# Kernel optimization log

Hardware: AMD Instinct MI355X
Metric: run time of the kernel (lower is better)

## Reference

```python
import jax, jax.numpy as jnp
import numpy as np

D_MODEL = 1024
H = 16
HEAD_DIM = D_MODEL // H  # 64


def setup_inputs() -> dict:
    key = jax.random.key(0)
    ks = jax.random.split(key, 11)
    B, S, D = 1, 4096, D_MODEL
    scale = 1.0 / np.sqrt(D)
    inp = {
        'q': jax.random.normal(ks[0], (B, S, D), jnp.float32),
        'k': jax.random.normal(ks[1], (B, S, D), jnp.float32),
        'v': jax.random.normal(ks[2], (B, S, D), jnp.float32),
        'w_q': jax.random.normal(ks[3], (D, D), jnp.float32) * scale,
        'b_q': jnp.zeros((D,), jnp.float32),
        'w_k': jax.random.normal(ks[4], (D, D), jnp.float32) * scale,
        'b_k': jnp.zeros((D,), jnp.float32),
        'w_v': jax.random.normal(ks[5], (D, D), jnp.float32) * scale,
        'b_v': jnp.zeros((D,), jnp.float32),
        'w_o': jax.random.normal(ks[6], (D, D), jnp.float32) * scale,
        'b_o': jnp.zeros((D,), jnp.float32),
    }
    return inp


def reference(q, k, v, w_q, b_q, w_k, b_k, w_v, b_v, w_o, b_o):
    B, Sq, D = q.shape
    Sk = k.shape[1]
    # Linear projections (torch Linear: x @ W.T + b), split into heads: [B,H,S,hd]
    Q = (q @ w_q.T + b_q).reshape(B, Sq, H, HEAD_DIM).transpose(0, 2, 1, 3)
    K = (k @ w_k.T + b_k).reshape(B, Sk, H, HEAD_DIM).transpose(0, 2, 1, 3)
    V = (v @ w_v.T + b_v).reshape(B, Sk, H, HEAD_DIM).transpose(0, 2, 1, 3)
    # Naive attention: full [B,H,Sq,Sk] scores, softmax, then AV
    scores = jnp.einsum('bhqd,bhkd->bhqk', Q, K) / jnp.sqrt(jnp.float32(HEAD_DIM))
    attn = jax.nn.softmax(scores, axis=-1)
    ctx = jnp.einsum('bhqk,bhkd->bhqd', attn, V)
    concat = ctx.transpose(0, 2, 1, 3).reshape(B, Sq, D)
    return concat @ w_o.T + b_o
```

## Files before the change

kernel.cpp:

```cpp
#include <hip/hip_runtime.h>
#include <stdint.h>

#define S_LEN 4096
#define DM 1024
#define NH 16

typedef __attribute__((ext_vector_type(8))) short short8;
typedef __attribute__((ext_vector_type(4))) float float4v;
typedef __attribute__((ext_vector_type(4))) unsigned short ushort4v;

typedef __attribute__((address_space(1))) const void* as1cvp;
typedef __attribute__((address_space(3))) void* as3vp;

#define MFMA16(a, b, c) __builtin_amdgcn_mfma_f32_16x16x32_bf16((a), (b), (c), 0, 0, 0)
#define GLOAD_LDS16(g, l) \
  __builtin_amdgcn_global_load_lds((as1cvp)(g), (as3vp)(l), 16, 0, 0)

__device__ __forceinline__ unsigned short f2bf(float f) {
  unsigned u = __float_as_uint(f);
  u += 0x7fffu + ((u >> 16) & 1u);
  return (unsigned short)(u >> 16);
}

__device__ __forceinline__ float exp2_hw(float x) {
  float r;
  asm("v_exp_f32 %0, %1" : "=v"(r) : "v"(x));
  return r;
}

__global__ __launch_bounds__(256) void cast_all(
    const float* __restrict__ q, const float* __restrict__ k, const float* __restrict__ v,
    const float* __restrict__ wq, const float* __restrict__ wk, const float* __restrict__ wv,
    const float* __restrict__ wo, unsigned short* __restrict__ dst)
{
  const float* src; size_t off; int n;
  switch (blockIdx.y) {
    case 0: src = q;  off = 0u;        n = 4194304; break;
    case 1: src = k;  off = 4194304u;  n = 4194304; break;
    case 2: src = v;  off = 8388608u;  n = 4194304; break;
    case 3: src = wq; off = 12582912u; n = 1048576; break;
    case 4: src = wk; off = 13631488u; n = 1048576; break;
    case 5: src = wv; off = 14680064u; n = 1048576; break;
    default: src = wo; off = 15728640u; n = 1048576; break;
  }
  int nv = n >> 2;
  for (int i = blockIdx.x * blockDim.x + threadIdx.x; i < nv; i += gridDim.x * blockDim.x) {
    float4v val = ((const float4v*)src)[i];
    ushort4v o;
    o.x = f2bf(val.x); o.y = f2bf(val.y); o.z = f2bf(val.z); o.w = f2bf(val.w);
    ((ushort4v*)(dst + off))[i] = o;
  }
}

template<int MODE>
__device__ __forceinline__ void gemm128(
    const unsigned short* __restrict__ A, const unsigned short* __restrict__ Bw,
    unsigned short* Cb, const float* __restrict__ bias, float alpha,
    unsigned short* As, unsigned short* Bs, unsigned short* T)
{
  const int K = 1024, N = 1024;
  int bm = blockIdx.x, bn = blockIdx.y;
  int t = threadIdx.x, lane = t & 63, w = t >> 6;
  int l15 = lane & 15, l4 = lane >> 4;
  int wr = w >> 1, wc = w & 1;

  float4v acc[4][4] = {};

  for (int kt = 0; kt < K / 64; ++kt) {
#pragma unroll
    for (int i = 0; i < 4; ++i) {
      int ci = i * 256 + t;
      int r = ci >> 3, cb = ci & 7;
      int lb = cb ^ (r & 7);
      GLOAD_LDS16(A + (size_t)(bm * 128 + r) * K + kt * 64 + lb * 8, As + (size_t)ci * 8);
      GLOAD_LDS16(Bw + (size_t)(bn * 128 + r) * K + kt * 64 + lb * 8, Bs + (size_t)ci * 8);
    }
    __syncthreads();
#pragma unroll
    for (int kk = 0; kk < 2; ++kk) {
      short8 af[4], bfr[4];
#pragma unroll
      for (int mf = 0; mf < 4; ++mf) {
        int row = wr * 64 + mf * 16 + l15;
        int pc = (kk * 4 + l4) ^ (row & 7);
        af[mf] = *(const short8*)&As[row * 64 + pc * 8];
      }
#pragma unroll
      for (int nf = 0; nf < 4; ++nf) {
        int row = wc * 64 + nf * 16 + l15;
        int pc = (kk * 4 + l4) ^ (row & 7);
        bfr[nf] = *(const short8*)&Bs[row * 64 + pc * 8];
      }
#pragma unroll
      for (int mf = 0; mf < 4; ++mf)
#pragma unroll
        for (int nf = 0; nf < 4; ++nf)
          acc[mf][nf] = MFMA16(af[mf], bfr[nf], acc[mf][nf]);
    }
    __syncthreads();
  }

  if (MODE == 2) {
#pragma unroll
    for (int hc = 0; hc < 2; ++hc) {
      if (wc == hc) {
#pragma unroll
        for (int mf = 0; mf < 4; ++mf)
#pragma unroll
          for (int nf = 0; nf < 4; ++nf) {
            int c = nf * 16 + l15;
            float bv = bias[bn * 128 + hc * 64 + c];
            ushort4v pk;
#pragma unroll
            for (int j = 0; j < 4; ++j) pk[j] = f2bf((acc[mf][nf][j] + bv) * alpha);
            *(ushort4v*)&T[c * 136 + wr * 64 + mf * 16 + l4 * 4] = pk;
          }
      }
      __syncthreads();
      {
        int c = t >> 2, rseg = (t & 3) * 32;
        size_t gbase = (size_t)(bn * 128 + hc * 64 + c) * S_LEN + bm * 128 + rseg;
#pragma unroll
        for (int s = 0; s < 4; ++s) {
          short8 vv = *(const short8*)&T[c * 136 + rseg + s * 8];
          *(short8*)&Cb[gbase + s * 8] = vv;
        }
      }
      __syncthreads();
    }
    return;
  }

#pragma unroll
  for (int mf = 0; mf < 4; ++mf)
#pragma unroll
    for (int nf = 0; nf < 4; ++nf) {
      int col = bn * 128 + wc * 64 + nf * 16 + l15;
      float bv = bias[col];
#pragma unroll
      for (int j = 0; j < 4; ++j) {
        int row = bm * 128 + wr * 64 + mf * 16 + l4 * 4 + j;
        Cb[(size_t)row * N + col] = f2bf((acc[mf][nf][j] + bv) * alpha);
      }
    }
}

__global__ __launch_bounds__(256) void proj_qkv(
    const unsigned short* xq, const unsigned short* xk, const unsigned short* xv,
    const unsigned short* wq, const unsigned short* wk, const unsigned short* wv,
    unsigned short* Qp, unsigned short* Kp, unsigned short* Vt,
    const float* bq, const float* bk, const float* bv)
{
  __shared__ unsigned short As[128 * 64], Bs[128 * 64];
  __shared__ unsigned short T[64 * 136];
  switch (blockIdx.z) {
    case 0:  gemm128<0>(xq, wq, Qp, bq, 0.1803368867f, As, Bs, T); break;
    case 1:  gemm128<0>(xk, wk, Kp, bk, 1.0f,          As, Bs, T); break;
    default: gemm128<2>(xv, wv, Vt, bv, 1.0f,          As, Bs, T); break;
  }
}

__global__ __launch_bounds__(256) void proj_o(
    const unsigned short* __restrict__ ctx, const unsigned short* __restrict__ wo,
    float* __restrict__ out, const float* __restrict__ bo)
{
  const int K = 1024, N = 1024;
  __shared__ unsigned short As[128 * 64], Bs[64 * 64];
  int bm = blockIdx.x, bn = blockIdx.y;
  int t = threadIdx.x, lane = t & 63, w = t >> 6;
  int l15 = lane & 15, l4 = lane >> 4;

  float4v acc[2][4] = {};

  for (int kt = 0; kt < K / 64; ++kt) {
#pragma unroll
    for (int i = 0; i < 4; ++i) {
      int ci = i * 256 + t;
      int r = ci >> 3, cb = ci & 7;
      int lb = cb ^ (r & 7);
      GLOAD_LDS16(ctx + (size_t)(bm * 128 + r) * K + kt * 64 + lb * 8, As + (size_t)ci * 8);
    }
#pragma unroll
    for (int i = 0; i < 2; ++i) {
      int ci = i * 256 + t;
      int r = ci >> 3, cb = ci & 7;
      int lb = cb ^ (r & 7);
      GLOAD_LDS16(wo + (size_t)(bn * 64 + r) * K + kt * 64 + lb * 8, Bs + (size_t)ci * 8);
    }
    __syncthreads();
#pragma unroll
    for (int kk = 0; kk < 2; ++kk) {
      short8 af[2], bfr[4];
#pragma unroll
      for (int mf = 0; mf < 2; ++mf) {
        int row = w * 32 + mf * 16 + l15;
        int pc = (kk * 4 + l4) ^ (row & 7);
        af[mf] = *(const short8*)&As[row * 64 + pc * 8];
      }
#pragma unroll
      for (int nf = 0; nf < 4; ++nf) {
        int row = nf * 16 + l15;
        int pc = (kk * 4 + l4) ^ (row & 7);
        bfr[nf] = *(const short8*)&Bs[row * 64 + pc * 8];
      }
#pragma unroll
      for (int mf = 0; mf < 2; ++mf)
#pragma unroll
        for (int nf = 0; nf < 4; ++nf)
          acc[mf][nf] = MFMA16(af[mf], bfr[nf], acc[mf][nf]);
    }
    __syncthreads();
  }

#pragma unroll
  for (int mf = 0; mf < 2; ++mf)
#pragma unroll
    for (int nf = 0; nf < 4; ++nf) {
      int col = bn * 64 + nf * 16 + l15;
      float bv = bo[col];
#pragma unroll
      for (int j = 0; j < 4; ++j) {
        int row = bm * 128 + w * 32 + mf * 16 + l4 * 4 + j;
        out[(size_t)row * N + col] = acc[mf][nf][j] + bv;
      }
    }
}

template<int BUF>
__device__ __forceinline__ void attn_tile(
    int kt,
    const unsigned short* kb0, const unsigned short* kb1,
    const unsigned short* vb0, const unsigned short* vb1,
    unsigned short* pw, const unsigned short* pr,
    const unsigned short* kg, const unsigned short* vg,
    unsigned short* kls, unsigned short* vls,
    const short8 (&qf)[2], float4v (&acc_o)[4], float& m_run, float& l_run,
    int l4)
{
  if (kt + 1 < 64) {
    GLOAD_LDS16(kg + (size_t)(kt + 1) * (64 * DM), kls + (1 - BUF) * 4096);
    GLOAD_LDS16(vg + (kt + 1) * 64, vls + (1 - BUF) * 4096);
  }

  float4v sc[4];
  __builtin_amdgcn_s_setprio(1);
#pragma unroll
  for (int nf = 0; nf < 4; ++nf) {
    short8 kf0 = *(const short8*)(kb0 + BUF * 4096 + nf * 1024);
    short8 kf1 = *(const short8*)(kb1 + BUF * 4096 + nf * 1024);
    float4v z = {0.f, 0.f, 0.f, 0.f};
    z = MFMA16(kf0, qf[0], z);
    sc[nf] = MFMA16(kf1, qf[1], z);
  }
  __builtin_amdgcn_s_setprio(0);

  float mxl = fmaxf(fmaxf(fmaxf(sc[0][0], sc[0][1]), sc[0][2]), sc[0][3]);
#pragma unroll
  for (int nf = 1; nf < 4; ++nf)
    mxl = fmaxf(fmaxf(fmaxf(fmaxf(mxl, sc[nf][0]), sc[nf][1]), sc[nf][2]), sc[nf][3]);

  if (!__all(mxl <= m_run + 11.5f)) {
    float mx = fmaxf(mxl, __shfl_xor(mxl, 16));
    mx = fmaxf(mx, __shfl_xor(mx, 32));
    float mnew = fmaxf(m_run, mx);
    float corr = exp2_hw(m_run - mnew);
    m_run = mnew;
    l_run *= corr;
#pragma unroll
    for (int j = 0; j < 4; ++j) {
      float cj = __shfl(corr, l4 * 4 + j);
#pragma unroll
      for (int nf2 = 0; nf2 < 4; ++nf2) acc_o[nf2][j] *= cj;
    }
  }

  float ps = 0.f;
#pragma unroll
  for (int nf = 0; nf < 4; ++nf) {
    float p0 = exp2_hw(sc[nf][0] - m_run);
    float p1 = exp2_hw(sc[nf][1] - m_run);
    float p2 = exp2_hw(sc[nf][2] - m_run);
    float p3 = exp2_hw(sc[nf][3] - m_run);
    ps += (p0 + p1) + (p2 + p3);
    unsigned lo, hi;
    asm("v_cvt_pk_bf16_f32 %0, %1, %2" : "=v"(lo) : "v"(p0), "v"(p1));
    asm("v_cvt_pk_bf16_f32 %0, %1, %2" : "=v"(hi) : "v"(p2), "v"(p3));
    uint2 u; u.x = lo; u.y = hi;
    *(uint2*)(pw + nf * 16) = u;
  }
  l_run += ps;

  short8 pf[2];
#pragma unroll
  for (int kc = 0; kc < 2; ++kc)
    pf[kc] = *(const short8*)(pr + kc * 32);

  __builtin_amdgcn_s_setprio(1);
#pragma unroll
  for (int nfd = 0; nfd < 4; ++nfd) {
    short8 vf0 = *(const short8*)(vb0 + BUF * 4096 + nfd * 1024);
    short8 vf1 = *(const short8*)(vb1 + BUF * 4096 + nfd * 1024);
    acc_o[nfd] = MFMA16(pf[0], vf0, acc_o[nfd]);
    acc_o[nfd] = MFMA16(pf[1], vf1, acc_o[nfd]);
  }
  __builtin_amdgcn_s_setprio(0);
  __syncthreads();
}

__global__ __launch_bounds__(512) void attn_fused(
    const unsigned short* __restrict__ Qp, const unsigned short* __restrict__ Kp,
    const unsigned short* __restrict__ Vt, unsigned short* __restrict__ ctx)
{
  __shared__ unsigned short Ks[2][64 * 64];
  __shared__ unsigned short Vts[2][64 * 64];
  __shared__ unsigned short Ps[8][16 * 72];

  int bid = blockIdx.x;
  int wg = (bid & 7) * 64 + (bid >> 3);
  int h = wg >> 5, qt = wg & 31;

  int t = threadIdx.x, lane = t & 63, w = t >> 6;
  int l15 = lane & 15, l4 = lane >> 4;

  short8 qf[2];
  int qrow0 = qt * 128 + w * 16;
#pragma unroll
  for (int ks = 0; ks < 2; ++ks)
    qf[ks] = *(const short8*)&Qp[(size_t)(qrow0 + l15) * DM + h * 64 + ks * 32 + l4 * 8];

  float4v acc_o[4] = {};
  float m_run = -INFINITY, l_run = 0.f;

  const int swz = l15 & 7;
  const unsigned short* kb0 = &Ks[0][l15 * 64 + ((l4) ^ swz) * 8];
  const unsigned short* kb1 = &Ks[0][l15 * 64 + ((4 + l4) ^ swz) * 8];
  const unsigned short* vb0 = &Vts[0][l15 * 64 + ((l4) ^ swz) * 8];
  const unsigned short* vb1 = &Vts[0][l15 * 64 + ((4 + l4) ^ swz) * 8];
  unsigned short* pw = &Ps[w][l15 * 72 + l4 * 4];
  const unsigned short* pr = &Ps[w][l15 * 72 + l4 * 8];

  int sr = t >> 3, sp = t & 7;
  int slb = sp ^ (sr & 7);
  const unsigned short* kg = Kp + (size_t)sr * DM + h * 64 + slb * 8;
  const unsigned short* vg = Vt + (size_t)(h * 64 + sr) * S_LEN + slb * 8;
  unsigned short* kls = &Ks[0][t * 8];
  unsigned short* vls = &Vts[0][t * 8];

  GLOAD_LDS16(kg, kls);
  GLOAD_LDS16(vg, vls);
  __syncthreads();

  for (int kt = 0; kt < 64; kt += 2) {
    attn_tile<0>(kt,     kb0, kb1, vb0, vb1, pw, pr, kg, vg, kls, vls, qf, acc_o, m_run, l_run, l4);
    attn_tile<1>(kt + 1, kb0, kb1, vb0, vb1, pw, pr, kg, vg, kls, vls, qf, acc_o, m_run, l_run, l4);
  }

  float lr = l_run;
  lr += __shfl_xor(lr, 16);
  lr += __shfl_xor(lr, 32);
#pragma unroll
  for (int j = 0; j < 4; ++j) {
    float lj = __shfl(lr, l4 * 4 + j);
    float inv = 1.0f / lj;
#pragma unroll
    for (int nfd = 0; nfd < 4; ++nfd) {
      int row = qrow0 + l4 * 4 + j;
      int col = h * 64 + nfd * 16 + l15;
      ctx[(size_t)row * DM + col] = f2bf(acc_o[nfd][j] * inv);
    }
  }
}

extern "C" void kernel_launch(void* const* d_in, const int* in_sizes, int n_in,
                              void* d_out, int out_size, void* d_ws, size_t ws_size,
                              hipStream_t stream) {
  const float* q  = (const float*)d_in[0];
  const float* k  = (const float*)d_in[1];
  const float* v  = (const float*)d_in[2];
  const float* wq = (const float*)d_in[3];
  const float* bq = (const float*)d_in[4];
  const float* wk = (const float*)d_in[5];
  const float* bk = (const float*)d_in[6];
  const float* wv = (const float*)d_in[7];
  const float* bv = (const float*)d_in[8];
  const float* wo = (const float*)d_in[9];
  const float* bo = (const float*)d_in[10];

  unsigned short* ws  = (unsigned short*)d_ws;
  unsigned short* qb  = ws;
  unsigned short* kb  = ws + 4194304u;
  unsigned short* vb  = ws + 8388608u;
  unsigned short* wqb = ws + 12582912u;
  unsigned short* wkb = ws + 13631488u;
  unsigned short* wvb = ws + 14680064u;
  unsigned short* wob = ws + 15728640u;
  unsigned short* Qp  = ws + 16777216u;
  unsigned short* Kp  = ws + 20971520u;
  unsigned short* Vt  = ws + 25165824u;
  unsigned short* ctx = qb;
  float* out = (float*)d_out;

  cast_all<<<dim3(1024, 7), 256, 0, stream>>>(q, k, v, wq, wk, wv, wo, ws);
  proj_qkv<<<dim3(32, 8, 3), 256, 0, stream>>>(qb, kb, vb, wqb, wkb, wvb, Qp, Kp, Vt, bq, bk, bv);
  attn_fused<<<dim3(512), 512, 0, stream>>>(Qp, Kp, Vt, ctx);
  proj_o<<<dim3(32, 16), 256, 0, stream>>>(ctx, wob, out, bo);
}
```

Baseline: 169.5 us.

## Quad-buffer K/V tiles to halve block barriers and swizzle P scratch layout

The K/V LDS staging grows from double to quad buffering. Two tiles are prefetched at a time and a block-wide barrier runs every two tiles instead of every tile, which cuts synchronisation overhead and gives loads more time to land. The per-wave P scratch drops its 72-element padding in favour of an XOR-swizzled 64-wide layout to avoid bank conflicts. LDS use roughly doubles for K/V, which could limit occupancy. P is now written and read within a wave without a barrier between tiles, which relies on wave-local ordering.

```diff
diff --git a/kernel.cpp b/kernel.cpp
--- a/kernel.cpp
+++ b/kernel.cpp
@@ -228,20 +228,13 @@
 
 template<int BUF>
 __device__ __forceinline__ void attn_tile(
-    int kt,
     const unsigned short* kb0, const unsigned short* kb1,
     const unsigned short* vb0, const unsigned short* vb1,
-    unsigned short* pw, const unsigned short* pr,
-    const unsigned short* kg, const unsigned short* vg,
-    unsigned short* kls, unsigned short* vls,
+    unsigned short* pwrow, const int (&pwo)[4],
+    const unsigned short* pr0, const unsigned short* pr1,
     const short8 (&qf)[2], float4v (&acc_o)[4], float& m_run, float& l_run,
     int l4)
 {
-  if (kt + 1 < 64) {
-    GLOAD_LDS16(kg + (size_t)(kt + 1) * (64 * DM), kls + (1 - BUF) * 4096);
-    GLOAD_LDS16(vg + (kt + 1) * 64, vls + (1 - BUF) * 4096);
-  }
-
   float4v sc[4];
   __builtin_amdgcn_s_setprio(1);
 #pragma unroll
@@ -286,14 +279,13 @@
     asm("v_cvt_pk_bf16_f32 %0, %1, %2" : "=v"(lo) : "v"(p0), "v"(p1));
     asm("v_cvt_pk_bf16_f32 %0, %1, %2" : "=v"(hi) : "v"(p2), "v"(p3));
     uint2 u; u.x = lo; u.y = hi;
-    *(uint2*)(pw + nf * 16) = u;
+    *(uint2*)(pwrow + pwo[nf]) = u;
   }
   l_run += ps;
 
   short8 pf[2];
-#pragma unroll
-  for (int kc = 0; kc < 2; ++kc)
-    pf[kc] = *(const short8*)(pr + kc * 32);
+  pf[0] = *(const short8*)pr0;
+  pf[1] = *(const short8*)pr1;
 
   __builtin_amdgcn_s_setprio(1);
 #pragma unroll
@@ -304,16 +296,15 @@
     acc_o[nfd] = MFMA16(pf[1], vf1, acc_o[nfd]);
   }
   __builtin_amdgcn_s_setprio(0);
-  __syncthreads();
 }
 
 __global__ __launch_bounds__(512) void attn_fused(
     const unsigned short* __restrict__ Qp, const unsigned short* __restrict__ Kp,
     const unsigned short* __restrict__ Vt, unsigned short* __restrict__ ctx)
 {
-  __shared__ unsigned short Ks[2][64 * 64];
-  __shared__ unsigned short Vts[2][64 * 64];
-  __shared__ unsigned short Ps[8][16 * 72];
+  __shared__ unsigned short Ks[4][64 * 64];
+  __shared__ unsigned short Vts[4][64 * 64];
+  __shared__ unsigned short Ps[8][16 * 64];
 
   int bid = blockIdx.x;
   int wg = (bid & 7) * 64 + (bid >> 3);
@@ -336,8 +327,13 @@
   const unsigned short* kb1 = &Ks[0][l15 * 64 + ((4 + l4) ^ swz) * 8];
   const unsigned short* vb0 = &Vts[0][l15 * 64 + ((l4) ^ swz) * 8];
   const unsigned short* vb1 = &Vts[0][l15 * 64 + ((4 + l4) ^ swz) * 8];
-  unsigned short* pw = &Ps[w][l15 * 72 + l4 * 4];
-  const unsigned short* pr = &Ps[w][l15 * 72 + l4 * 8];
+  unsigned short* pwrow = &Ps[w][l15 * 64];
+  int pwo[4];
+#pragma unroll
+  for (int nf = 0; nf < 4; ++nf)
+    pwo[nf] = ((2 * nf + (l4 >> 1)) ^ swz) * 8 + (l4 & 1) * 4;
+  const unsigned short* pr0 = &Ps[w][l15 * 64 + ((l4) ^ swz) * 8];
+  const unsigned short* pr1 = &Ps[w][l15 * 64 + ((4 + l4) ^ swz) * 8];
 
   int sr = t >> 3, sp = t & 7;
   int slb = sp ^ (sr & 7);
@@ -346,14 +342,28 @@
   unsigned short* kls = &Ks[0][t * 8];
   unsigned short* vls = &Vts[0][t * 8];
 
-  GLOAD_LDS16(kg, kls);
-  GLOAD_LDS16(vg, vls);
+#define STAGE_T(BUFI, ktv) do {                                      \
+    GLOAD_LDS16(kg + (size_t)(ktv) * (64 * DM), kls + (BUFI) * 4096); \
+    GLOAD_LDS16(vg + (ktv) * 64,                vls + (BUFI) * 4096); \
+  } while (0)
+
+  STAGE_T(0, 0);
+  STAGE_T(1, 1);
   __syncthreads();
 
-  for (int kt = 0; kt < 64; kt += 2) {
-    attn_tile<0>(kt,     kb0, kb1, vb0, vb1, pw, pr, kg, vg, kls, vls, qf, acc_o, m_run, l_run, l4);
-    attn_tile<1>(kt + 1, kb0, kb1, vb0, vb1, pw, pr, kg, vg, kls, vls, qf, acc_o, m_run, l_run, l4);
-  }
+  for (int kt = 0; kt < 64; kt += 4) {
+    if (kt + 2 < 64) STAGE_T(2, kt + 2);
+    if (kt + 3 < 64) STAGE_T(3, kt + 3);
+    attn_tile<0>(kb0, kb1, vb0, vb1, pwrow, pwo, pr0, pr1, qf, acc_o, m_run, l_run, l4);
+    attn_tile<1>(kb0, kb1, vb0, vb1, pwrow, pwo, pr0, pr1, qf, acc_o, m_run, l_run, l4);
+    __syncthreads();
+    if (kt + 4 < 64) STAGE_T(0, kt + 4);
+    if (kt + 5 < 64) STAGE_T(1, kt + 5);
+    attn_tile<2>(kb0, kb1, vb0, vb1, pwrow, pwo, pr0, pr1, qf, acc_o, m_run, l_run, l4);
+    attn_tile<3>(kb0, kb1, vb0, vb1, pwrow, pwo, pr0, pr1, qf, acc_o, m_run, l_run, l4);
+    __syncthreads();
+  }
+#undef STAGE_T
 
   float lr = l_run;
   lr += __shfl_xor(lr, 16);
```

Measured after the change: 167.7 us. No clear change (-1.1%).
